# Kernel tuning notes

Measured on AMD Instinct MI355X. Metric: run time of the kernel, lower is better.

Reference implementation:

```python
import jax, jax.numpy as jnp
import numpy as np

D_MODEL = 1024
NUM_HEADS = 16
HEAD_DIM = D_MODEL // NUM_HEADS


def setup_inputs() -> dict:
    key = jax.random.key(0)
    ks = jax.random.split(key, 7)
    B, S = 4, 2048
    scale = 1.0 / np.sqrt(D_MODEL)
    x = jax.random.normal(ks[0], (B, S, D_MODEL), dtype=jnp.float32)
    Wq = jax.random.normal(ks[1], (D_MODEL, D_MODEL), dtype=jnp.float32) * scale
    Wk = jax.random.normal(ks[2], (D_MODEL, D_MODEL), dtype=jnp.float32) * scale
    Wv = jax.random.normal(ks[3], (D_MODEL, D_MODEL), dtype=jnp.float32) * scale
    bq = jax.random.normal(ks[4], (D_MODEL,), dtype=jnp.float32) * 0.02
    bk = jax.random.normal(ks[5], (D_MODEL,), dtype=jnp.float32) * 0.02
    bv = jax.random.normal(ks[6], (D_MODEL,), dtype=jnp.float32) * 0.02
    return {"x": x, "Wq": Wq, "bq": bq, "Wk": Wk, "bk": bk, "Wv": Wv, "bv": bv}


def reference(x, Wq, bq, Wk, bk, Wv, bv):
    B, S, _ = x.shape
    # QKV projections (nn.Linear: x @ W^T + b; here W stored as [in, out] already)
    q = x @ Wq + bq
    k = x @ Wk + bk
    v = x @ Wv + bv
    # [B, H, S, Dh]
    def split_heads(t):
        return t.reshape(B, S, NUM_HEADS, HEAD_DIM).transpose(0, 2, 1, 3)
    q, k, v = split_heads(q), split_heads(k), split_heads(v)
    # NOTE: module scales by sqrt(d_model), NOT sqrt(head_dim)
    scores = jnp.einsum("bhqd,bhkd->bhqk", q, k) / jnp.sqrt(jnp.float32(D_MODEL))
    attn = jax.nn.softmax(scores, axis=-1)  # dropout = identity (eval mode)
    out = jnp.einsum("bhqk,bhkd->bhqd", attn, v)
    return out.transpose(0, 2, 1, 3).reshape(B, S, D_MODEL)
```

## Files before the change

### kernel.cpp

```cpp
#include <hip/hip_runtime.h>


typedef __attribute__((ext_vector_type(8))) __bf16 bf16x8;
typedef __attribute__((ext_vector_type(8))) unsigned short ushort8;
typedef __attribute__((ext_vector_type(4))) float floatx4;

#if __has_builtin(__builtin_amdgcn_exp2f)
#define EXP2(x) __builtin_amdgcn_exp2f(x)
#else
#define EXP2(x) __expf((x) * 0.6931471805599453f)
#endif

__device__ __forceinline__ unsigned short f2bf(float f) {
    __bf16 h = (__bf16)f;
    return __builtin_bit_cast(unsigned short, h);
}
__device__ __forceinline__ bf16x8 pack8(floatx4 a, floatx4 b) {
    bf16x8 v = {(__bf16)a[0], (__bf16)a[1], (__bf16)a[2], (__bf16)a[3],
                (__bf16)b[0], (__bf16)b[1], (__bf16)b[2], (__bf16)b[3]};
    return v;
}
__device__ __forceinline__ floatx4 mfma16(bf16x8 a, bf16x8 b, floatx4 c) {
    return __builtin_amdgcn_mfma_f32_16x16x32_bf16(a, b, c, 0, 0, 0);
}
__device__ __forceinline__ int spos(int s) {
    int rk = s & 31;
    return (s & ~31) | (((rk & 15) >> 2) * 8 + ((rk >> 4) << 2) + (rk & 3));
}
__device__ __forceinline__ void glds16(const void* g, void* l) {
    __builtin_amdgcn_global_load_lds(
        (const __attribute__((address_space(1))) unsigned int*)g,
        (__attribute__((address_space(3))) unsigned int*)l, 16, 0, 0);
}

__global__ __launch_bounds__(256) void prep_all(
    const float* __restrict__ X, unsigned short* __restrict__ Xb,
    const float* __restrict__ Wq, const float* __restrict__ Wk,
    const float* __restrict__ Wv,
    unsigned short* __restrict__ WqT, unsigned short* __restrict__ WkT,
    unsigned short* __restrict__ WvT) {
    __shared__ unsigned short Ls[64 * 72];
    const int tid = threadIdx.x, bx = blockIdx.x;
    if (bx < 4096) {
        int i = (bx * 256 + tid) * 8;
        float4 a = *(const float4*)&X[i];
        float4 b = *(const float4*)&X[i + 4];
        bf16x8 v = {(__bf16)a.x, (__bf16)a.y, (__bf16)a.z, (__bf16)a.w,
                    (__bf16)b.x, (__bf16)b.y, (__bf16)b.z, (__bf16)b.w};
        *(bf16x8*)&Xb[i] = v;
        return;
    }
    const int idx4 = bx - 4096;
    const int z = idx4 >> 8, xx = idx4 & 255;
    const float* W = (z == 0) ? Wq : (z == 1) ? Wk : Wv;
    unsigned short* WT = (z == 0) ? WqT : (z == 1) ? WkT : WvT;
    const int k0 = (xx >> 4) * 64, o0 = (xx & 15) * 64;
#pragma unroll
    for (int e = 0; e < 4; ++e) {
        int idx = e * 256 + tid;
        int r = idx >> 4, c = (idx & 15) * 4;
        float4 f = *(const float4*)&W[(size_t)(k0 + r) * 1024 + o0 + c];
        Ls[(c + 0) * 72 + r] = f2bf(f.x);
        Ls[(c + 1) * 72 + r] = f2bf(f.y);
        Ls[(c + 2) * 72 + r] = f2bf(f.z);
        Ls[(c + 3) * 72 + r] = f2bf(f.w);
    }
    __syncthreads();
#pragma unroll
    for (int e = 0; e < 2; ++e) {
        int idx = e * 256 + tid;
        int rr = idx >> 3, ch = (idx & 7) * 8;
        *(ushort8*)&WT[(size_t)(o0 + rr) * 1024 + k0 + ch] =
            *(const ushort8*)&Ls[rr * 72 + ch];
    }
}

__global__ __launch_bounds__(256, 3) void qkv_gemm(
    const unsigned short* __restrict__ Xb,
    const unsigned short* __restrict__ WqT,
    const unsigned short* __restrict__ WkT,
    const unsigned short* __restrict__ WvT,
    const float* __restrict__ bq, const float* __restrict__ bk,
    const float* __restrict__ bv,
    unsigned short* __restrict__ Kh, unsigned short* __restrict__ Vt,
    float* __restrict__ Qs_out) {

    __shared__ __align__(16) unsigned char arena[32768];

    const int tid = threadIdx.x;
    const int w = tid >> 6, lane = tid & 63;
    const int l15 = lane & 15, quad = lane >> 4;
    const int z = blockIdx.z;
    const int tok_base = blockIdx.x * 128, o_base = blockIdx.y * 128;
    const int wr = w >> 1, wc = w & 1;

    const unsigned short* Wsrc = (z == 0) ? WkT : (z == 1) ? WvT : WqT;
    const char* Asrc = (z == 1) ? (const char*)(Wsrc + (size_t)o_base * 1024)
                                : (const char*)(Xb + (size_t)tok_base * 1024);
    const char* Bsrc = (z == 1) ? (const char*)(Xb + (size_t)tok_base * 1024)
                                : (const char*)(Wsrc + (size_t)o_base * 1024);

    const int coff = (((lane & 7) ^ (lane >> 3)) << 4);
    const char* pa[4];
    const char* pb[4];
    unsigned char* la[4];
    unsigned char* lb[4];
#pragma unroll
    for (int e = 0; e < 4; ++e) {
        int r = (e * 4 + w) * 8 + (lane >> 3);
        pa[e] = Asrc + (size_t)r * 2048 + coff;
        pb[e] = Bsrc + (size_t)r * 2048 + coff;
        la[e] = arena + (e * 4 + w) * 1024;
        lb[e] = arena + 16384 + (e * 4 + w) * 1024;
    }

    const unsigned cq = (unsigned)((quad ^ (l15 & 7)) << 4);
    unsigned offA[4], offB[4];
#pragma unroll
    for (int t = 0; t < 4; ++t) {
        offA[t] = (unsigned)((wr * 64 + t * 16 + l15) * 128) + cq;
        offB[t] = 16384u + (unsigned)((wc * 64 + t * 16 + l15) * 128) + cq;
    }

    floatx4 acc[4][4];
#pragma unroll
    for (int mt = 0; mt < 4; ++mt)
#pragma unroll
        for (int nt = 0; nt < 4; ++nt) acc[mt][nt] = (floatx4){0.f, 0.f, 0.f, 0.f};

    for (int k0 = 0; k0 < 1024; k0 += 64) {
        __syncthreads();
#pragma unroll
        for (int e = 0; e < 4; ++e) {
            glds16(pa[e], la[e]);
            glds16(pb[e], lb[e]);
            pa[e] += 128;
            pb[e] += 128;
        }
        __syncthreads();

#pragma unroll
        for (int kc = 0; kc < 2; ++kc) {
            bf16x8 af[4], bfr[4];
#pragma unroll
            for (int mt = 0; mt < 4; ++mt)
                af[mt] = *(const bf16x8*)&arena[offA[mt] ^ (unsigned)(kc << 6)];
#pragma unroll
            for (int nt = 0; nt < 4; ++nt)
                bfr[nt] = *(const bf16x8*)&arena[offB[nt] ^ (unsigned)(kc << 6)];
#pragma unroll
            for (int mt = 0; mt < 4; ++mt)
#pragma unroll
                for (int nt = 0; nt < 4; ++nt)
                    acc[mt][nt] = mfma16(af[mt], bfr[nt], acc[mt][nt]);
        }
    }

    if (z == 0) {
#pragma unroll
        for (int nt = 0; nt < 4; ++nt) {
            int col = o_base + wc * 64 + nt * 16 + l15;
            float bia = bk[col];
            int h = col >> 6, dh = col & 63;
#pragma unroll
            for (int mt = 0; mt < 4; ++mt)
#pragma unroll
                for (int r = 0; r < 4; ++r) {
                    int t = tok_base + wr * 64 + mt * 16 + quad * 4 + r;
                    int bb = t >> 11, s = t & 2047;
                    Kh[(((size_t)(bb * 16 + h)) * 2048 + s) * 64 + dh] =
                        f2bf(acc[mt][nt][r] + bia);
                }
        }
    } else if (z == 1) {
#pragma unroll
        for (int mt = 0; mt < 4; ++mt)
#pragma unroll
            for (int r = 0; r < 4; ++r) {
                int o = o_base + wr * 64 + mt * 16 + quad * 4 + r;
                float bia = bv[o];
#pragma unroll
                for (int nt = 0; nt < 4; ++nt) {
                    int t = tok_base + wc * 64 + nt * 16 + l15;
                    int bb = t >> 11, s = t & 2047;
                    Vt[((size_t)(bb * 1024 + o)) * 2048 + spos(s)] =
                        f2bf(acc[mt][nt][r] + bia);
                }
            }
    } else {
        const float QS = 0.03125f * 1.44269504f;
        unsigned short* Qb = (unsigned short*)Qs_out;
#pragma unroll
        for (int nt = 0; nt < 4; ++nt) {
            int col = o_base + wc * 64 + nt * 16 + l15;
            float bia = bq[col];
            int h = col >> 6, d = col & 63;
#pragma unroll
            for (int mt = 0; mt < 4; ++mt)
#pragma unroll
                for (int r = 0; r < 4; ++r) {
                    int t = tok_base + wr * 64 + mt * 16 + quad * 4 + r;
                    Qb[(size_t)t * 2048 + h * 128 + d] =
                        f2bf((acc[mt][nt][r] + bia) * QS);
                }
        }
    }
}

__global__ __launch_bounds__(256, 4) void attn_kernel(
    const unsigned short* __restrict__ Kh,
    const unsigned short* __restrict__ Vt,
    float* __restrict__ out) {

    __shared__ __align__(16) unsigned char arena[32768];

    const int tid = threadIdx.x;
    const int w = tid >> 6, lane = tid & 63;
    const int l15 = lane & 15, quad = lane >> 4;
    const int qb = blockIdx.x, h = blockIdx.y, b = blockIdx.z;
    const size_t head_elems = ((size_t)(b * 16 + h)) * 2048 * 64;

    const unsigned short* Qb = (const unsigned short*)out;
    bf16x8 aq[2][2];
#pragma unroll
    for (int g = 0; g < 2; ++g)
#pragma unroll
        for (int kc = 0; kc < 2; ++kc) {
            int q = b * 2048 + qb * 128 + w * 32 + g * 16 + l15;
            aq[g][kc] = *(const bf16x8*)
                &Qb[(size_t)q * 2048 + h * 128 + kc * 32 + quad * 8];
        }
    __builtin_amdgcn_sched_barrier(0);

    const int coff = (((lane & 7) ^ (lane >> 3)) << 4);
    const char* pk[2];
    const char* pv[2];
    unsigned char* lk[2];
    unsigned char* lv[2];
#pragma unroll
    for (int e = 0; e < 2; ++e) {
        int r = (e * 4 + w) * 8 + (lane >> 3);
        pk[e] = (const char*)Kh + head_elems * 2 + (size_t)r * 128 + coff;
        pv[e] = (const char*)Vt + ((size_t)(b * 1024 + h * 64 + r)) * 4096 + coff;
        lk[e] = arena + (e * 4 + w) * 1024;
        lv[e] = arena + 8192 + (e * 4 + w) * 1024;
    }
    auto stage = [&](int bufsel) {
        int bo = bufsel << 14;
#pragma unroll
        for (int e = 0; e < 2; ++e) {
            glds16(pk[e], lk[e] + bo);
            glds16(pv[e], lv[e] + bo);
            pk[e] += 8192;
            pv[e] += 128;
        }
    };

    unsigned kb[4], vb[4];
#pragma unroll
    for (int t = 0; t < 4; ++t) {
        int rk = t * 16 + l15;
        unsigned sw = (unsigned)((quad ^ (rk & 7)) << 4);
        kb[t] = (unsigned)(rk * 128) + sw;
        vb[t] = 8192u + (unsigned)(rk * 128) + sw;
    }

    const bf16x8 ONES = {(__bf16)1.f, (__bf16)1.f, (__bf16)1.f, (__bf16)1.f,
                         (__bf16)1.f, (__bf16)1.f, (__bf16)1.f, (__bf16)1.f};
    floatx4 lacc[2];
    floatx4 O[2][4];
#pragma unroll
    for (int g = 0; g < 2; ++g) {
        lacc[g] = (floatx4){0.f, 0.f, 0.f, 0.f};
#pragma unroll
        for (int n4 = 0; n4 < 4; ++n4) O[g][n4] = (floatx4){0.f, 0.f, 0.f, 0.f};
    }

    stage(0);

#pragma unroll 1
    for (int kt = 0; kt < 32; ++kt) {
        if (kt < 31) {
            stage((kt + 1) & 1);
            asm volatile("s_waitcnt vmcnt(4)" ::: "memory");
        } else {
            asm volatile("s_waitcnt vmcnt(0)" ::: "memory");
        }
        __builtin_amdgcn_s_barrier();
        const unsigned bsel = (unsigned)((kt & 1) << 14);

        floatx4 s0[2][2], s1[2][2];
        __builtin_amdgcn_s_setprio(1);
#pragma unroll
        for (int kg = 0; kg < 2; ++kg)
#pragma unroll
            for (int mm = 0; mm < 2; ++mm) {
                int m16 = 2 * kg + mm;
                unsigned ka = kb[m16] ^ bsel;
                bf16x8 kf0 = *(const bf16x8*)&arena[ka];
                bf16x8 kf1 = *(const bf16x8*)&arena[ka ^ 64u];
#pragma unroll
                for (int g = 0; g < 2; ++g) {
                    floatx4 a0 = (floatx4){0.f, 0.f, 0.f, 0.f};
                    a0 = mfma16(kf0, aq[g][0], a0);
                    a0 = mfma16(kf1, aq[g][1], a0);
                    if (mm == 0) s0[kg][g] = a0; else s1[kg][g] = a0;
                }
            }
        __builtin_amdgcn_s_setprio(0);

        bf16x8 ap[2][2];
#pragma unroll
        for (int kg = 0; kg < 2; ++kg)
#pragma unroll
            for (int g = 0; g < 2; ++g) {
                floatx4 p0, p1;
#pragma unroll
                for (int r = 0; r < 4; ++r) {
                    p0[r] = EXP2(s0[kg][g][r]);
                    p1[r] = EXP2(s1[kg][g][r]);
                }
                ap[g][kg] = pack8(p0, p1);
                lacc[g] = mfma16(ap[g][kg], ONES, lacc[g]);
            }

        __builtin_amdgcn_s_setprio(1);
#pragma unroll
        for (int n4 = 0; n4 < 4; ++n4)
#pragma unroll
            for (int kg = 0; kg < 2; ++kg) {
                bf16x8 vf = *(const bf16x8*)
                    &arena[(vb[n4] ^ bsel) ^ (unsigned)(kg << 6)];
#pragma unroll
                for (int g = 0; g < 2; ++g)
                    O[g][n4] = mfma16(ap[g][kg], vf, O[g][n4]);
            }
        __builtin_amdgcn_s_setprio(0);

        asm volatile("s_waitcnt lgkmcnt(0)" ::: "memory");
        __builtin_amdgcn_s_barrier();
    }

#pragma unroll
    for (int g = 0; g < 2; ++g)
#pragma unroll
        for (int r = 0; r < 4; ++r) {
            float inv = 1.f / lacc[g][r];
            int srow = qb * 128 + w * 32 + g * 16 + quad * 4 + r;
#pragma unroll
            for (int n4 = 0; n4 < 4; ++n4)
                out[((size_t)(b * 2048 + srow)) * 1024 + h * 64 + n4 * 16 + l15] =
                    O[g][n4][r] * inv;
        }
}

extern "C" void kernel_launch(void* const* d_in, const int* in_sizes, int n_in,
                              void* d_out, int out_size, void* d_ws, size_t ws_size,
                              hipStream_t stream) {
    const float *x, *Wq, *bq, *Wk, *bk, *Wv, *bv;
    x = (const float*)d_in[0];
    if (in_sizes[2] == 1024) {
        Wq = (const float*)d_in[1];  bq = (const float*)d_in[2];
        Wk = (const float*)d_in[3];  bk = (const float*)d_in[4];
        Wv = (const float*)d_in[5];  bv = (const float*)d_in[6];
    } else {
        Wq = (const float*)d_in[1];  Wk = (const float*)d_in[2];
        Wv = (const float*)d_in[3];
        bq = (const float*)d_in[4];  bk = (const float*)d_in[5];
        bv = (const float*)d_in[6];
    }
    float* out = (float*)d_out;

    char* ws = (char*)d_ws;
    unsigned short* Xb  = (unsigned short*)(ws);
    unsigned short* Kh  = (unsigned short*)(ws + (16u << 20));
    unsigned short* Vt  = (unsigned short*)(ws + (32u << 20));
    unsigned short* WqT = (unsigned short*)(ws + (48u << 20));
    unsigned short* WkT = (unsigned short*)(ws + (50u << 20));
    unsigned short* WvT = (unsigned short*)(ws + (52u << 20));

    prep_all<<<4864, 256, 0, stream>>>(x, Xb, Wq, Wk, Wv, WqT, WkT, WvT);
    qkv_gemm<<<dim3(64, 8, 3), 256, 0, stream>>>(Xb, WqT, WkT, WvT, bq, bk, bv,
                                                 Kh, Vt, out);
    attn_kernel<<<dim3(16, 16, 4), 256, 0, stream>>>(Kh, Vt, out);
}
```

Measured before the change: 217.8 us.

## Multi-stage pipeline QKV GEMM global-to-LDS loads with 4-buffer ring

Restructures the QKV projection GEMM main loop from a synchronous single-buffer load/compute pattern into a 4-slot LDS ring buffer. K-tiles of 32 are prefetched three steps ahead, with vmcnt-based waits and a single barrier per iteration. MFMA sections are given raised wave priority. LDS use doubles to 64KB and the occupancy hint drops from 3 to 2 blocks per CU, trading occupancy for latency hiding.

Result: slower. 224.6 us (+3.1%).

```diff
diff --git a/kernel.cpp b/kernel.cpp
--- a/kernel.cpp
+++ b/kernel.cpp
@@ -75,7 +75,7 @@
     }
 }
 
-__global__ __launch_bounds__(256, 3) void qkv_gemm(
+__global__ __launch_bounds__(256, 2) void qkv_gemm(
     const unsigned short* __restrict__ Xb,
     const unsigned short* __restrict__ WqT,
     const unsigned short* __restrict__ WkT,
@@ -85,7 +85,7 @@
     unsigned short* __restrict__ Kh, unsigned short* __restrict__ Vt,
     float* __restrict__ Qs_out) {
 
-    __shared__ __align__(16) unsigned char arena[32768];
+    __shared__ __align__(16) unsigned char arena[65536];
 
     const int tid = threadIdx.x;
     const int w = tid >> 6, lane = tid & 63;
@@ -100,26 +100,35 @@
     const char* Bsrc = (z == 1) ? (const char*)(Xb + (size_t)tok_base * 1024)
                                 : (const char*)(Wsrc + (size_t)o_base * 1024);
 
-    const int coff = (((lane & 7) ^ (lane >> 3)) << 4);
-    const char* pa[4];
-    const char* pb[4];
-    unsigned char* la[4];
-    unsigned char* lb[4];
-#pragma unroll
-    for (int e = 0; e < 4; ++e) {
-        int r = (e * 4 + w) * 8 + (lane >> 3);
-        pa[e] = Asrc + (size_t)r * 2048 + coff;
-        pb[e] = Bsrc + (size_t)r * 2048 + coff;
-        la[e] = arena + (e * 4 + w) * 1024;
-        lb[e] = arena + 16384 + (e * 4 + w) * 1024;
-    }
-
-    const unsigned cq = (unsigned)((quad ^ (l15 & 7)) << 4);
+    const int coff = (((lane & 3) ^ ((lane >> 3) & 3)) << 4);
+    const char* pa[2];
+    const char* pb[2];
+    unsigned la_off[2], lb_off[2];
+#pragma unroll
+    for (int e = 0; e < 2; ++e) {
+        int seg = e * 4 + w;
+        size_t roff = (size_t)(seg * 16 + (lane >> 2)) * 2048 + coff;
+        pa[e] = Asrc + roff;
+        pb[e] = Bsrc + roff;
+        la_off[e] = (unsigned)(seg * 1024);
+        lb_off[e] = 8192u + (unsigned)(seg * 1024);
+    }
+    auto stage = [&](int t) {
+        unsigned char* base = arena + ((t & 3) << 14);
+        size_t ko = (size_t)t * 64;
+#pragma unroll
+        for (int e = 0; e < 2; ++e) {
+            glds16(pa[e] + ko, base + la_off[e]);
+            glds16(pb[e] + ko, base + lb_off[e]);
+        }
+    };
+
+    const unsigned cq = (unsigned)((quad ^ ((l15 >> 1) & 3)) << 4);
     unsigned offA[4], offB[4];
 #pragma unroll
     for (int t = 0; t < 4; ++t) {
-        offA[t] = (unsigned)((wr * 64 + t * 16 + l15) * 128) + cq;
-        offB[t] = 16384u + (unsigned)((wc * 64 + t * 16 + l15) * 128) + cq;
+        offA[t] = (unsigned)((wr * 64 + t * 16 + l15) * 64) + cq;
+        offB[t] = 8192u + (unsigned)((wc * 64 + t * 16 + l15) * 64) + cq;
     }
 
     floatx4 acc[4][4];
@@ -128,32 +137,37 @@
 #pragma unroll
         for (int nt = 0; nt < 4; ++nt) acc[mt][nt] = (floatx4){0.f, 0.f, 0.f, 0.f};
 
-    for (int k0 = 0; k0 < 1024; k0 += 64) {
-        __syncthreads();
-#pragma unroll
-        for (int e = 0; e < 4; ++e) {
-            glds16(pa[e], la[e]);
-            glds16(pb[e], lb[e]);
-            pa[e] += 128;
-            pb[e] += 128;
-        }
-        __syncthreads();
-
-#pragma unroll
-        for (int kc = 0; kc < 2; ++kc) {
-            bf16x8 af[4], bfr[4];
-#pragma unroll
-            for (int mt = 0; mt < 4; ++mt)
-                af[mt] = *(const bf16x8*)&arena[offA[mt] ^ (unsigned)(kc << 6)];
+    stage(0);
+    stage(1);
+    stage(2);
+
+#pragma unroll 1
+    for (int t = 0; t < 32; ++t) {
+        if (t < 30) {
+            asm volatile("s_waitcnt vmcnt(8)" ::: "memory");
+        } else if (t == 30) {
+            asm volatile("s_waitcnt vmcnt(4)" ::: "memory");
+        } else {
+            asm volatile("s_waitcnt vmcnt(0)" ::: "memory");
+        }
+        __builtin_amdgcn_s_barrier();
+        if (t < 29) stage(t + 3);
+
+        const unsigned sb = (unsigned)((t & 3) << 14);
+        bf16x8 af[4], bfr[4];
+#pragma unroll
+        for (int mt = 0; mt < 4; ++mt)
+            af[mt] = *(const bf16x8*)&arena[sb + offA[mt]];
+#pragma unroll
+        for (int nt = 0; nt < 4; ++nt)
+            bfr[nt] = *(const bf16x8*)&arena[sb + offB[nt]];
+        __builtin_amdgcn_s_setprio(1);
+#pragma unroll
+        for (int mt = 0; mt < 4; ++mt)
 #pragma unroll
             for (int nt = 0; nt < 4; ++nt)
-                bfr[nt] = *(const bf16x8*)&arena[offB[nt] ^ (unsigned)(kc << 6)];
-#pragma unroll
-            for (int mt = 0; mt < 4; ++mt)
-#pragma unroll
-                for (int nt = 0; nt < 4; ++nt)
-                    acc[mt][nt] = mfma16(af[mt], bfr[nt], acc[mt][nt]);
-        }
+                acc[mt][nt] = mfma16(af[mt], bfr[nt], acc[mt][nt]);
+        __builtin_amdgcn_s_setprio(0);
     }
 
     if (z == 0) {
```
